# Kernel optimization log

Hardware: AMD Instinct MI355X
Metric: run time of the kernel (lower is better)

The kernel has to match this reference:

```python
import jax, jax.numpy as jnp
import numpy as np

V, D, H, HS, BLK, L = 50257, 768, 12, 64, 1024, 6
B, S = 4, 1024
EPS = 1e-5


def layer_norm(x, g, b):
    mu = jnp.mean(x, axis=-1, keepdims=True)
    var = jnp.mean(jnp.square(x - mu), axis=-1, keepdims=True)
    return (x - mu) * jax.lax.rsqrt(var + EPS) * g + b


def setup_inputs() -> dict:
    key = jax.random.key(0)
    ks = jax.random.split(key, 24)
    s = 0.02
    inp = {
        "idx": jax.random.randint(ks[0], (B, S), 0, V),
        "tok_emb": jax.random.normal(ks[1], (V, D), jnp.float32) * s,
        "pos_emb": jax.random.normal(ks[2], (BLK, D), jnp.float32) * s,
        "Wq": jax.random.normal(ks[3], (L, H, D, HS), jnp.float32) * s,
        "bq": jnp.zeros((L, H, HS), jnp.float32),
        "Wk": jax.random.normal(ks[4], (L, H, D, HS), jnp.float32) * s,
        "bk": jnp.zeros((L, H, HS), jnp.float32),
        "Wv": jax.random.normal(ks[5], (L, H, D, HS), jnp.float32) * s,
        "bv": jnp.zeros((L, H, HS), jnp.float32),
        "Wproj": jax.random.normal(ks[6], (L, D, D), jnp.float32) * s,
        "bproj": jnp.zeros((L, D), jnp.float32),
        "ln1_g": jnp.ones((L, D), jnp.float32),
        "ln1_b": jnp.zeros((L, D), jnp.float32),
        "ln2_g": jnp.ones((L, D), jnp.float32),
        "ln2_b": jnp.zeros((L, D), jnp.float32),
        "Wf1": jax.random.normal(ks[7], (L, D, 4 * D), jnp.float32) * s,
        "bf1": jnp.zeros((L, 4 * D), jnp.float32),
        "Wf2": jax.random.normal(ks[8], (L, 4 * D, D), jnp.float32) * s,
        "bf2": jnp.zeros((L, D), jnp.float32),
        "lnf_g": jnp.ones((D,), jnp.float32),
        "lnf_b": jnp.zeros((D,), jnp.float32),
        "Wlm": jax.random.normal(ks[9], (V, D), jnp.float32) * s,
    }
    return inp


def attention(x, Wq, bq, Wk, bk, Wv, bv, Wproj, bproj):
    # x: [B,S,D]; per-head projections stacked over H
    q = jnp.einsum("bsd,hdk->bhsk", x, Wq) + bq[:, None, :]
    k = jnp.einsum("bsd,hdk->bhsk", x, Wk) + bk[:, None, :]
    v = jnp.einsum("bsd,hdk->bhsk", x, Wv) + bv[:, None, :]
    scores = jnp.einsum("bhsk,bhtk->bhst", q, k)  # [B,H,S,S]
    s = x.shape[1]
    mask = jnp.tril(jnp.ones((s, s), bool))
    # original: masked_fill(-inf) THEN divide by sqrt(head_size) -- equivalent
    scores = jnp.where(mask, scores, -jnp.inf) / np.sqrt(HS)
    w = jax.nn.softmax(scores, axis=-1)
    out = jnp.einsum("bhst,bhtk->bhsk", w, v)
    out = out.transpose(0, 2, 1, 3).reshape(x.shape[0], s, H * HS)
    return out @ Wproj + bproj


def reference(idx, tok_emb, pos_emb, Wq, bq, Wk, bk, Wv, bv, Wproj, bproj,
              ln1_g, ln1_b, ln2_g, ln2_b, Wf1, bf1, Wf2, bf2, lnf_g, lnf_b, Wlm):
    s = idx.shape[1]
    x = tok_emb[idx] + pos_emb[:s]
    for i in range(L):
        h = layer_norm(x, ln1_g[i], ln1_b[i])
        x = x + attention(h, Wq[i], bq[i], Wk[i], bk[i], Wv[i], bv[i], Wproj[i], bproj[i])
        h = layer_norm(x, ln2_g[i], ln2_b[i])
        x = x + (jax.nn.gelu(h @ Wf1[i] + bf1[i], approximate=False) @ Wf2[i] + bf2[i])
    x = layer_norm(x, lnf_g, lnf_b)
    logits = x @ Wlm.T  # [B,S,V]
    return logits
```

## Files before the change

### kernel.cpp

```cpp
#include <hip/hip_runtime.h>
#include <hip/hip_bf16.h>
#include <math.h>

#define D_MODEL 768
#define N_HEAD  12
#define HEAD    64
#define SEQ     1024
#define NLAYER  6
#define BATCH   4
#define NROWS   (BATCH*SEQ)
#define VOCAB   50257
#define VPAD    50432
#define DFFN    3072
#define DQKV    2304

typedef __attribute__((ext_vector_type(8))) __bf16 bf16x8;
typedef __attribute__((ext_vector_type(4))) float f32x4;
typedef __attribute__((ext_vector_type(4))) unsigned short u16x4;

__device__ inline unsigned short f2bf(float x) {
    __hip_bfloat16 h = __float2bfloat16(x);
    return *reinterpret_cast<unsigned short*>(&h);
}

__global__ __launch_bounds__(256)
void embed_kernel(const int* __restrict__ idx, const float* __restrict__ tok,
                  const float* __restrict__ pos, float* __restrict__ x) {
    int row = blockIdx.x;
    int t = idx[row];
    int s = row & (SEQ - 1);
    const float* tp = tok + (size_t)t * D_MODEL;
    const float* pp = pos + (size_t)s * D_MODEL;
    float* xp = x + (size_t)row * D_MODEL;
    for (int i = threadIdx.x; i < D_MODEL; i += 256) xp[i] = tp[i] + pp[i];
}

__global__ __launch_bounds__(256)
void ln_kernel(const float* __restrict__ in, const float* __restrict__ gw,
               const float* __restrict__ bw, unsigned short* __restrict__ out) {
    int row = blockIdx.x;
    int tid = threadIdx.x;
    const float* x = in + (size_t)row * D_MODEL;
    float v0 = x[tid], v1 = x[tid + 256], v2 = x[tid + 512];
    float s  = v0 + v1 + v2;
    float sq = v0*v0 + v1*v1 + v2*v2;
    #pragma unroll
    for (int o = 1; o < 64; o <<= 1) { s += __shfl_xor(s, o); sq += __shfl_xor(sq, o); }
    __shared__ float red[8];
    int wave = tid >> 6;
    if ((tid & 63) == 0) { red[wave] = s; red[4 + wave] = sq; }
    __syncthreads();
    s  = red[0] + red[1] + red[2] + red[3];
    sq = red[4] + red[5] + red[6] + red[7];
    float mean = s * (1.0f / D_MODEL);
    float var  = sq * (1.0f / D_MODEL) - mean * mean;
    float rstd = rsqrtf(var + 1e-5f);
    unsigned short* op = out + (size_t)row * D_MODEL;
    op[tid]       = f2bf((v0 - mean) * rstd * gw[tid]       + bw[tid]);
    op[tid + 256] = f2bf((v1 - mean) * rstd * gw[tid + 256] + bw[tid + 256]);
    op[tid + 512] = f2bf((v2 - mean) * rstd * gw[tid + 512] + bw[tid + 512]);
}

template<int MODE>
__global__ __launch_bounds__(256)
void conv_transpose(const float* __restrict__ in, unsigned short* __restrict__ out,
                    int K, int N, size_t inLstride, size_t outLstride) {
    __shared__ float t[32][33];
    const int tx = threadIdx.x, ty = threadIdx.y;
    const int n0 = blockIdx.x * 32, k0 = blockIdx.y * 32;
    const float* ip = in + blockIdx.z * inLstride;
    unsigned short* op = out + blockIdx.z * outLstride;
    #pragma unroll
    for (int j = 0; j < 4; ++j) {
        int k = k0 + ty + j * 8, n = n0 + tx;
        float v = (MODE == 0) ? ip[(size_t)k * N + n]
                              : ip[(size_t)((n >> 6) * K + k) * 64 + (n & 63)];
        t[ty + j * 8][tx] = v;
    }
    __syncthreads();
    #pragma unroll
    for (int j = 0; j < 4; ++j) {
        int n = n0 + ty + j * 8, k = k0 + tx;
        op[(size_t)n * K + k] = f2bf(t[tx][ty + j * 8]);
    }
}

__global__ __launch_bounds__(256)
void conv_lm(const float* __restrict__ in, unsigned short* __restrict__ out) {
    const int nchunks = VPAD * D_MODEL / 4;
    const int vchunks = VOCAB * D_MODEL / 4;
    for (int i = blockIdx.x * 256 + threadIdx.x; i < nchunks; i += gridDim.x * 256) {
        u16x4 o;
        if (i < vchunks) {
            float4 v = reinterpret_cast<const float4*>(in)[i];
            o[0] = f2bf(v.x); o[1] = f2bf(v.y); o[2] = f2bf(v.z); o[3] = f2bf(v.w);
        } else { o[0] = 0; o[1] = 0; o[2] = 0; o[3] = 0; }
        reinterpret_cast<u16x4*>(out)[i] = o;
    }
}

__global__ __launch_bounds__(256)
void conv_bias(const float* __restrict__ bq, const float* __restrict__ bk,
               const float* __restrict__ bv, float* __restrict__ out) {
    int i = blockIdx.x * 256 + threadIdx.x;
    if (i >= NLAYER * DQKV) return;
    int l = i / DQKV, n = i % DQKV;
    float v;
    if (n < 768)        v = bq[l * 768 + n];
    else if (n < 1536)  v = bk[l * 768 + n - 768];
    else                v = bv[l * 768 + n - 1536];
    out[i] = v;
}

__global__ __launch_bounds__(512)
void gemm256_mfma(const unsigned short* __restrict__ A, const unsigned short* __restrict__ B,
                  float* __restrict__ C, int M, int N, int K) {
    __shared__ unsigned short smem[2 * 2 * 16384];
    const int nwg = gridDim.x;
    const int t0 = (blockIdx.x & 7) * (nwg >> 3) + (blockIdx.x >> 3);
    const int MT = M >> 8;
    const int NBX = nwg / MT;
    const int srsize = NBX * 8;
    const int sr = t0 / srsize;
    const int rem = t0 - sr * srsize;
    const int bx = rem >> 3;
    const int by = sr * 8 + (rem & 7);
    const int bm = by * 256, bn = bx * 256;
    const int tid = threadIdx.x;
    const int l = tid & 63, w = tid >> 6;
    const int wm = w >> 2, wn = w & 3;
    const int lr = l & 15, lc = l >> 4;
    f32x4 acc[8][4] = {};

    auto stage = [&](int k0, int buf) {
        #pragma unroll
        for (int p = 0; p < 4; ++p) {
            int d16 = p * 512 + tid;
            int row = d16 >> 3, cph = d16 & 7;
            int clog = cph ^ (row & 7);
            const unsigned short* ga = A + (size_t)(bm + row) * K + k0 + clog * 8;
            __builtin_amdgcn_global_load_lds(
                (const __attribute__((address_space(1))) unsigned int*)ga,
                (__attribute__((address_space(3))) unsigned int*)(&smem[buf * 32768 + d16 * 8]), 16, 0, 0);
        }
        #pragma unroll
        for (int p = 0; p < 4; ++p) {
            int d16 = p * 512 + tid;
            int row = d16 >> 3, cph = d16 & 7;
            int clog = cph ^ (row & 7);
            const unsigned short* gb = B + (size_t)(bn + row) * K + k0 + clog * 8;
            __builtin_amdgcn_global_load_lds(
                (const __attribute__((address_space(1))) unsigned int*)gb,
                (__attribute__((address_space(3))) unsigned int*)(&smem[buf * 32768 + 16384 + d16 * 8]), 16, 0, 0);
        }
    };

    auto compute = [&](int buf) {
        const unsigned short* Ab = &smem[buf * 32768];
        const unsigned short* Bb = &smem[buf * 32768 + 16384];
        #pragma unroll
        for (int qm = 0; qm < 2; ++qm) {
            bf16x8 af[2][4];
            #pragma unroll
            for (int ks = 0; ks < 2; ++ks)
                #pragma unroll
                for (int mi = 0; mi < 4; ++mi) {
                    int row = wm * 128 + qm * 64 + mi * 16 + lr;
                    af[ks][mi] = *reinterpret_cast<const bf16x8*>(
                        &Ab[row * 64 + (((ks * 4 + lc) ^ (row & 7)) * 8)]);
                }
            #pragma unroll
            for (int qn = 0; qn < 2; ++qn) {
                bf16x8 bfr[2][2];
                #pragma unroll
                for (int ks = 0; ks < 2; ++ks)
                    #pragma unroll
                    for (int ni = 0; ni < 2; ++ni) {
                        int col = wn * 64 + qn * 32 + ni * 16 + lr;
                        bfr[ks][ni] = *reinterpret_cast<const bf16x8*>(
                            &Bb[col * 64 + (((ks * 4 + lc) ^ (col & 7)) * 8)]);
                    }
                __builtin_amdgcn_s_setprio(1);
                #pragma unroll
                for (int ks = 0; ks < 2; ++ks)
                    #pragma unroll
                    for (int mi = 0; mi < 4; ++mi)
                        #pragma unroll
                        for (int ni = 0; ni < 2; ++ni)
                            acc[qm * 4 + mi][qn * 2 + ni] = __builtin_amdgcn_mfma_f32_16x16x32_bf16(
                                af[ks][mi], bfr[ks][ni], acc[qm * 4 + mi][qn * 2 + ni], 0, 0, 0);
                __builtin_amdgcn_s_setprio(0);
            }
        }
    };

    const int NT = K >> 6;
    stage(0, 0);
    asm volatile("s_waitcnt vmcnt(0)" ::: "memory");
    __builtin_amdgcn_s_barrier();
    for (int t = 0; t < NT; ++t) {
        const int cur = t & 1;
        if (t + 1 < NT) stage((t + 1) << 6, cur ^ 1);
        compute(cur);
        if (t + 1 < NT) {
            asm volatile("s_waitcnt vmcnt(0)" ::: "memory");
            __builtin_amdgcn_s_barrier();
        }
    }

    #pragma unroll
    for (int i = 0; i < 8; ++i) {
        #pragma unroll
        for (int r = 0; r < 4; ++r) {
            const int row = bm + wm * 128 + i * 16 + lc * 4 + r;
            #pragma unroll
            for (int j = 0; j < 4; ++j) {
                const int col = bn + wn * 64 + j * 16 + lr;
                if (col < N) C[(size_t)row * N + col] = acc[i][j][r];
            }
        }
    }
}

template<int OUTF , bool GELU, bool RES>
__global__ __launch_bounds__(256)
void gemm128p(const unsigned short* __restrict__ A, const unsigned short* __restrict__ B,
              const float* __restrict__ bias, const float* __restrict__ res,
              void* __restrict__ Cout, int M, int N, int K) {
    __shared__ unsigned short smem[2 * 2 * 8192];
    const int nwg = gridDim.x;
    const int t0 = (blockIdx.x & 7) * (nwg >> 3) + (blockIdx.x >> 3);
    const int MT = M >> 7;
    const int NBX = nwg / MT;
    const int srsize = NBX * 8;
    const int sr = t0 / srsize;
    const int rem = t0 - sr * srsize;
    const int bx = rem >> 3;
    const int by = sr * 8 + (rem & 7);
    const int bm = by * 128, bn = bx * 128;
    const int tid = threadIdx.x;
    const int l = tid & 63, w = tid >> 6;
    const int wr = (w >> 1) * 64, wc = (w & 1) * 64;
    const int lr = l & 15, lc = l >> 4;
    f32x4 acc[4][4] = {};

    auto stage = [&](int k0, int buf) {
        #pragma unroll
        for (int p = 0; p < 4; ++p) {
            int d16 = p * 256 + tid;
            int row = d16 >> 3, cph = d16 & 7;
            int clog = cph ^ (row & 7);
            const unsigned short* ga = A + (size_t)(bm + row) * K + k0 + clog * 8;
            __builtin_amdgcn_global_load_lds(
                (const __attribute__((address_space(1))) unsigned int*)ga,
                (__attribute__((address_space(3))) unsigned int*)(&smem[buf * 16384 + d16 * 8]), 16, 0, 0);
        }
        #pragma unroll
        for (int p = 0; p < 4; ++p) {
            int d16 = p * 256 + tid;
            int row = d16 >> 3, cph = d16 & 7;
            int clog = cph ^ (row & 7);
            const unsigned short* gb = B + (size_t)(bn + row) * K + k0 + clog * 8;
            __builtin_amdgcn_global_load_lds(
                (const __attribute__((address_space(1))) unsigned int*)gb,
                (__attribute__((address_space(3))) unsigned int*)(&smem[buf * 16384 + 8192 + d16 * 8]), 16, 0, 0);
        }
    };

    auto compute = [&](int buf) {
        const unsigned short* Ab = &smem[buf * 16384];
        const unsigned short* Bb = &smem[buf * 16384 + 8192];
        #pragma unroll
        for (int ks = 0; ks < 2; ++ks) {
            bf16x8 af[4], bfr[4];
            #pragma unroll
            for (int mi = 0; mi < 4; ++mi) {
                int row = wr + mi * 16 + lr;
                af[mi] = *reinterpret_cast<const bf16x8*>(
                    &Ab[row * 64 + (((ks * 4 + lc) ^ (row & 7)) * 8)]);
            }
            #pragma unroll
            for (int ni = 0; ni < 4; ++ni) {
                int col = wc + ni * 16 + lr;
                bfr[ni] = *reinterpret_cast<const bf16x8*>(
                    &Bb[col * 64 + (((ks * 4 + lc) ^ (col & 7)) * 8)]);
            }
            __builtin_amdgcn_s_setprio(1);
            #pragma unroll
            for (int mi = 0; mi < 4; ++mi)
                #pragma unroll
                for (int ni = 0; ni < 4; ++ni)
                    acc[mi][ni] = __builtin_amdgcn_mfma_f32_16x16x32_bf16(
                        af[mi], bfr[ni], acc[mi][ni], 0, 0, 0);
            __builtin_amdgcn_s_setprio(0);
        }
    };

    const int NT = K >> 6;
    stage(0, 0);
    asm volatile("s_waitcnt vmcnt(0)" ::: "memory");
    __builtin_amdgcn_s_barrier();
    for (int t = 0; t < NT; ++t) {
        const int cur = t & 1;
        if (t + 1 < NT) stage((t + 1) << 6, cur ^ 1);
        compute(cur);
        if (t + 1 < NT) {
            asm volatile("s_waitcnt vmcnt(0)" ::: "memory");
            __builtin_amdgcn_s_barrier();
        }
    }

    #pragma unroll
    for (int mi = 0; mi < 4; ++mi) {
        #pragma unroll
        for (int r = 0; r < 4; ++r) {
            const int row = bm + wr + mi * 16 + lc * 4 + r;
            #pragma unroll
            for (int ni = 0; ni < 4; ++ni) {
                const int col = bn + wc + ni * 16 + lr;
                float v = acc[mi][ni][r];
                if (bias) v += bias[col];
                if (GELU) v = 0.5f * v * (1.0f + erff(v * 0.70710678118654752f));
                if (RES)  v += res[(size_t)row * N + col];
                if (OUTF == 0) ((float*)Cout)[(size_t)row * N + col] = v;
                else ((unsigned short*)Cout)[(size_t)row * N + col] = f2bf(v);
            }
        }
    }
}

__global__ __launch_bounds__(256)
void attn_mfma(const unsigned short* __restrict__ qkv, unsigned short* __restrict__ ao) {
    const int qt = gridDim.x - 1 - blockIdx.x;
    const int h = blockIdx.y, b = blockIdx.z;
    const int tid = threadIdx.x;
    const int w = tid >> 6, l = tid & 63;
    const int c = l & 15, g = l >> 4;

    __shared__ unsigned short Ks[32 * 64];
    __shared__ unsigned short Vt[64 * 40];
    __shared__ unsigned int   Ps[4][16 * 20];

    const unsigned short* base = qkv + (size_t)(b * SEQ) * DQKV + h * HEAD;
    const int q0 = qt * 64 + w * 16;

    bf16x8 qf[2];
    {
        const unsigned short* qp = base + (size_t)(q0 + c) * DQKV + g * 8;
        qf[0] = *reinterpret_cast<const bf16x8*>(qp);
        qf[1] = *reinterpret_cast<const bf16x8*>(qp + 32);
    }

    f32x4 o_acc[4] = {};
    float m_run[4]  = {-INFINITY, -INFINITY, -INFINITY, -INFINITY};
    float l_run[4]  = {0.f, 0.f, 0.f, 0.f};

    const int srow = tid >> 3, schunk = tid & 7;
    const int vd = tid & 63, vw = tid >> 6;

    const int nkt = 2 * qt + 2;
    for (int kt = 0; kt < nkt; ++kt) {
        {
            const unsigned short* kp = base + (size_t)(kt * 32 + srow) * DQKV + 768 + schunk * 8;
            bf16x8 kv = *reinterpret_cast<const bf16x8*>(kp);
            *reinterpret_cast<bf16x8*>(&Ks[srow * 64 + ((schunk ^ (srow & 7)) * 8)]) = kv;
        }
        {
            unsigned short vv[8];
            #pragma unroll
            for (int j = 0; j < 8; ++j)
                vv[j] = base[(size_t)(kt * 32 + vw * 8 + j) * DQKV + 1536 + vd];
            uint4 pk;
            pk.x = vv[0] | ((unsigned)vv[1] << 16);
            pk.y = vv[2] | ((unsigned)vv[3] << 16);
            pk.z = vv[4] | ((unsigned)vv[5] << 16);
            pk.w = vv[6] | ((unsigned)vv[7] << 16);
            *reinterpret_cast<uint4*>(&Vt[vd * 40 + vw * 8]) = pk;
        }
        __syncthreads();

        f32x4 s_acc[2] = {};
        #pragma unroll
        for (int t = 0; t < 2; ++t) {
            const int kr = t * 16 + c;
            #pragma unroll
            for (int ks = 0; ks < 2; ++ks) {
                bf16x8 kf = *reinterpret_cast<const bf16x8*>(
                    &Ks[kr * 64 + (((ks * 4 + g) ^ (kr & 7)) * 8)]);
                s_acc[t] = __builtin_amdgcn_mfma_f32_16x16x32_bf16(qf[ks], kf, s_acc[t], 0, 0, 0);
            }
        }
        float sc[2][4];
        #pragma unroll
        for (int t = 0; t < 2; ++t) {
            const int kglob = kt * 32 + t * 16 + c;
            #pragma unroll
            for (int r = 0; r < 4; ++r) {
                float v = s_acc[t][r] * 0.125f;
                sc[t][r] = (kglob > q0 + g * 4 + r) ? -1e30f : v;
            }
        }
        float pout[2][4];
        #pragma unroll
        for (int r = 0; r < 4; ++r) {
            float tmax = fmaxf(sc[0][r], sc[1][r]);
            #pragma unroll
            for (int ms = 1; ms < 16; ms <<= 1) tmax = fmaxf(tmax, __shfl_xor(tmax, ms));
            float mnew = fmaxf(m_run[r], tmax);
            float alpha = __expf(m_run[r] - mnew);
            float p0 = __expf(sc[0][r] - mnew);
            float p1 = __expf(sc[1][r] - mnew);
            float psum = p0 + p1;
            #pragma unroll
            for (int ms = 1; ms < 16; ms <<= 1) psum += __shfl_xor(psum, ms);
            l_run[r] = l_run[r] * alpha + psum;
            m_run[r] = mnew;
            #pragma unroll
            for (int dt = 0; dt < 4; ++dt) o_acc[dt][r] *= alpha;
            pout[0][r] = p0; pout[1][r] = p1;
        }
        #pragma unroll
        for (int t = 0; t < 2; ++t) {
            #pragma unroll
            for (int r = 0; r < 4; ++r) {
                int my = f2bf(pout[t][r]);
                int part = __shfl_xor(my, 1);
                unsigned int word = (c & 1) ? ((unsigned)(part & 0xffff) | ((unsigned)my << 16))
                                            : ((unsigned)(my & 0xffff) | ((unsigned)part << 16));
                Ps[w][(g * 4 + r) * 20 + t * 8 + (c >> 1)] = word;
            }
        }
        uint4 praw = *reinterpret_cast<const uint4*>(&Ps[w][c * 20 + g * 4]);
        bf16x8 pf = *reinterpret_cast<const bf16x8*>(&praw);
        #pragma unroll
        for (int dt = 0; dt < 4; ++dt) {
            bf16x8 vf = *reinterpret_cast<const bf16x8*>(&Vt[(dt * 16 + c) * 40 + g * 8]);
            o_acc[dt] = __builtin_amdgcn_mfma_f32_16x16x32_bf16(pf, vf, o_acc[dt], 0, 0, 0);
        }
        __syncthreads();
    }

    float inv[4];
    #pragma unroll
    for (int r = 0; r < 4; ++r) inv[r] = 1.0f / l_run[r];
    #pragma unroll
    for (int r = 0; r < 4; ++r) {
        unsigned short* op = ao + (size_t)(b * SEQ + q0 + g * 4 + r) * D_MODEL + h * HEAD + c;
        #pragma unroll
        for (int dt = 0; dt < 4; ++dt)
            op[dt * 16] = f2bf(o_acc[dt][r] * inv[r]);
    }
}

extern "C" void kernel_launch(void* const* d_in, const int* in_sizes, int n_in,
                              void* d_out, int out_size, void* d_ws, size_t ws_size,
                              hipStream_t stream) {
    const int*   idx     = (const int*)  d_in[0];
    const float* tok_emb = (const float*)d_in[1];
    const float* pos_emb = (const float*)d_in[2];
    const float* Wq      = (const float*)d_in[3];
    const float* bq      = (const float*)d_in[4];
    const float* Wk      = (const float*)d_in[5];
    const float* bk      = (const float*)d_in[6];
    const float* Wv      = (const float*)d_in[7];
    const float* bv      = (const float*)d_in[8];
    const float* Wproj   = (const float*)d_in[9];
    const float* bproj   = (const float*)d_in[10];
    const float* ln1g    = (const float*)d_in[11];
    const float* ln1b    = (const float*)d_in[12];
    const float* ln2g    = (const float*)d_in[13];
    const float* ln2b    = (const float*)d_in[14];
    const float* Wf1     = (const float*)d_in[15];
    const float* bf1     = (const float*)d_in[16];
    const float* Wf2     = (const float*)d_in[17];
    const float* bf2     = (const float*)d_in[18];
    const float* lnfg    = (const float*)d_in[19];
    const float* lnfb    = (const float*)d_in[20];
    const float* Wlm     = (const float*)d_in[21];
    float* outp = (float*)d_out;

    char* basep = (char*)d_ws;
    size_t off = 0;
    auto alloc = [&](size_t bytes) -> void* {
        void* p = basep + off;
        off = (off + bytes + 255) & ~(size_t)255;
        return p;
    };
    float*          x      = (float*)         alloc((size_t)NROWS * D_MODEL * 4);
    unsigned short* qkv    = (unsigned short*)alloc((size_t)NROWS * DQKV * 2);
    unsigned short* hb     = (unsigned short*)alloc((size_t)NROWS * D_MODEL * 2);
    unsigned short* ao     = (unsigned short*)alloc((size_t)NROWS * D_MODEL * 2);
    unsigned short* mid    = (unsigned short*)alloc((size_t)NROWS * DFFN * 2);
    unsigned short* Wqkvb  = (unsigned short*)alloc((size_t)NLAYER * DQKV * D_MODEL * 2);
    unsigned short* Wprojb = (unsigned short*)alloc((size_t)NLAYER * D_MODEL * D_MODEL * 2);
    unsigned short* Wf1b   = (unsigned short*)alloc((size_t)NLAYER * DFFN * D_MODEL * 2);
    unsigned short* Wf2b   = (unsigned short*)alloc((size_t)NLAYER * D_MODEL * DFFN * 2);
    unsigned short* Wlmb   = (unsigned short*)alloc((size_t)VPAD * D_MODEL * 2);
    float*          bqkv   = (float*)         alloc((size_t)NLAYER * DQKV * 4);

    dim3 blk(256);
    dim3 tblk(32, 8);

    conv_lm<<<2048, blk, 0, stream>>>(Wlm, Wlmb);
    conv_transpose<1><<<dim3(24, 24, 6), tblk, 0, stream>>>(Wq, Wqkvb,             768, 768,  (size_t)768*768,  (size_t)DQKV*768);
    conv_transpose<1><<<dim3(24, 24, 6), tblk, 0, stream>>>(Wk, Wqkvb + 768*768,   768, 768,  (size_t)768*768,  (size_t)DQKV*768);
    conv_transpose<1><<<dim3(24, 24, 6), tblk, 0, stream>>>(Wv, Wqkvb + 2*768*768, 768, 768,  (size_t)768*768,  (size_t)DQKV*768);
    conv_transpose<0><<<dim3(24, 24, 6), tblk, 0, stream>>>(Wproj, Wprojb,         768, 768,  (size_t)768*768,  (size_t)768*768);
    conv_transpose<0><<<dim3(96, 24, 6), tblk, 0, stream>>>(Wf1, Wf1b,             768, 3072, (size_t)768*3072, (size_t)3072*768);
    conv_transpose<0><<<dim3(24, 96, 6), tblk, 0, stream>>>(Wf2, Wf2b,             3072, 768, (size_t)3072*768, (size_t)768*3072);
    conv_bias<<<(NLAYER * DQKV + 255) / 256, blk, 0, stream>>>(bq, bk, bv, bqkv);

    embed_kernel<<<NROWS, blk, 0, stream>>>(idx, tok_emb, pos_emb, x);

    dim3 gqkv(32 * 18);
    dim3 g768(32 * 6);
    dim3 g3072(32 * 24);
    dim3 ga(SEQ / 64, N_HEAD, BATCH);

    for (int li = 0; li < NLAYER; ++li) {
        ln_kernel<<<NROWS, blk, 0, stream>>>(x, ln1g + li * D_MODEL, ln1b + li * D_MODEL, hb);

        gemm128p<1, false, false><<<gqkv, blk, 0, stream>>>(
            hb, Wqkvb + (size_t)li * DQKV * D_MODEL, bqkv + li * DQKV, nullptr,
            qkv, NROWS, DQKV, D_MODEL);

        attn_mfma<<<ga, blk, 0, stream>>>(qkv, ao);

        gemm128p<0, false, true><<<g768, blk, 0, stream>>>(
            ao, Wprojb + (size_t)li * D_MODEL * D_MODEL, bproj + li * D_MODEL, x,
            x, NROWS, D_MODEL, D_MODEL);

        ln_kernel<<<NROWS, blk, 0, stream>>>(x, ln2g + li * D_MODEL, ln2b + li * D_MODEL, hb);

        gemm128p<1, true, false><<<g3072, blk, 0, stream>>>(
            hb, Wf1b + (size_t)li * DFFN * D_MODEL, bf1 + li * DFFN, nullptr,
            mid, NROWS, DFFN, D_MODEL);

        gemm128p<0, false, true><<<g768, blk, 0, stream>>>(
            mid, Wf2b + (size_t)li * D_MODEL * DFFN, bf2 + li * D_MODEL, x,
            x, NROWS, D_MODEL, DFFN);
    }

    ln_kernel<<<NROWS, blk, 0, stream>>>(x, lnfg, lnfb, hb);

    dim3 gl((VPAD / 256) * (NROWS / 256));
    gemm256_mfma<<<gl, dim3(512), 0, stream>>>(hb, Wlmb, outp, NROWS, VOCAB, D_MODEL);
}
```

Baseline: 2.336 ms.

## Use 64-row tiles for N=768 GEMMs and 512-thread attention blocks

Templates the GEMM on the M tile size. The two N=768 residual GEMMs (proj and FFN2) now use 64x128 tiles, which doubles the workgroup count from 192 to 384 and fills more CUs. Attention blocks grow to 8 waves covering 128 query rows, so each K/V tile staged in shared memory is reused by twice as many queries. Each thread now loads half-width K/V chunks. The cost is more causal-mask waste per block and smaller per-wave MFMA tiles in the 64-row GEMM.

```diff
diff --git a/kernel.cpp b/kernel.cpp
--- a/kernel.cpp
+++ b/kernel.cpp
@@ -222,38 +222,42 @@
     }
 }
 
-template<int OUTF , bool GELU, bool RES>
+template<int BM, int OUTF , bool GELU, bool RES>
 __global__ __launch_bounds__(256)
-void gemm128p(const unsigned short* __restrict__ A, const unsigned short* __restrict__ B,
-              const float* __restrict__ bias, const float* __restrict__ res,
-              void* __restrict__ Cout, int M, int N, int K) {
-    __shared__ unsigned short smem[2 * 2 * 8192];
+void gemm_sched(const unsigned short* __restrict__ A, const unsigned short* __restrict__ B,
+                const float* __restrict__ bias, const float* __restrict__ res,
+                void* __restrict__ Cout, int M, int N, int K) {
+    constexpr int ABUF = BM * 64;
+    constexpr int TBUF = (BM + 128) * 64;
+    __shared__ unsigned short smem[2 * TBUF];
     const int nwg = gridDim.x;
     const int t0 = (blockIdx.x & 7) * (nwg >> 3) + (blockIdx.x >> 3);
-    const int MT = M >> 7;
+    const int MT = M / BM;
     const int NBX = nwg / MT;
     const int srsize = NBX * 8;
     const int sr = t0 / srsize;
     const int rem = t0 - sr * srsize;
     const int bx = rem >> 3;
     const int by = sr * 8 + (rem & 7);
-    const int bm = by * 128, bn = bx * 128;
+    const int bm = by * BM, bn = bx * 128;
     const int tid = threadIdx.x;
     const int l = tid & 63, w = tid >> 6;
-    const int wr = (w >> 1) * 64, wc = (w & 1) * 64;
+    constexpr int MI = (BM == 128) ? 4 : 2;
+    const int wr = (BM == 128) ? (w >> 1) * 64 : (w & 1) * 32;
+    const int wc = (BM == 128) ? (w & 1) * 64 : (w >> 1) * 64;
     const int lr = l & 15, lc = l >> 4;
-    f32x4 acc[4][4] = {};
+    f32x4 acc[MI][4] = {};
 
     auto stage = [&](int k0, int buf) {
         #pragma unroll
-        for (int p = 0; p < 4; ++p) {
+        for (int p = 0; p < BM * 8 / 256; ++p) {
             int d16 = p * 256 + tid;
             int row = d16 >> 3, cph = d16 & 7;
             int clog = cph ^ (row & 7);
             const unsigned short* ga = A + (size_t)(bm + row) * K + k0 + clog * 8;
             __builtin_amdgcn_global_load_lds(
                 (const __attribute__((address_space(1))) unsigned int*)ga,
-                (__attribute__((address_space(3))) unsigned int*)(&smem[buf * 16384 + d16 * 8]), 16, 0, 0);
+                (__attribute__((address_space(3))) unsigned int*)(&smem[buf * TBUF + d16 * 8]), 16, 0, 0);
         }
         #pragma unroll
         for (int p = 0; p < 4; ++p) {
@@ -263,18 +267,18 @@
             const unsigned short* gb = B + (size_t)(bn + row) * K + k0 + clog * 8;
             __builtin_amdgcn_global_load_lds(
                 (const __attribute__((address_space(1))) unsigned int*)gb,
-                (__attribute__((address_space(3))) unsigned int*)(&smem[buf * 16384 + 8192 + d16 * 8]), 16, 0, 0);
+                (__attribute__((address_space(3))) unsigned int*)(&smem[buf * TBUF + ABUF + d16 * 8]), 16, 0, 0);
         }
     };
 
     auto compute = [&](int buf) {
-        const unsigned short* Ab = &smem[buf * 16384];
-        const unsigned short* Bb = &smem[buf * 16384 + 8192];
+        const unsigned short* Ab = &smem[buf * TBUF];
+        const unsigned short* Bb = &smem[buf * TBUF + ABUF];
         #pragma unroll
         for (int ks = 0; ks < 2; ++ks) {
-            bf16x8 af[4], bfr[4];
-            #pragma unroll
-            for (int mi = 0; mi < 4; ++mi) {
+            bf16x8 af[MI], bfr[4];
+            #pragma unroll
+            for (int mi = 0; mi < MI; ++mi) {
                 int row = wr + mi * 16 + lr;
                 af[mi] = *reinterpret_cast<const bf16x8*>(
                     &Ab[row * 64 + (((ks * 4 + lc) ^ (row & 7)) * 8)]);
@@ -287,7 +291,7 @@
             }
             __builtin_amdgcn_s_setprio(1);
             #pragma unroll
-            for (int mi = 0; mi < 4; ++mi)
+            for (int mi = 0; mi < MI; ++mi)
                 #pragma unroll
                 for (int ni = 0; ni < 4; ++ni)
                     acc[mi][ni] = __builtin_amdgcn_mfma_f32_16x16x32_bf16(
@@ -311,7 +315,7 @@
     }
 
     #pragma unroll
-    for (int mi = 0; mi < 4; ++mi) {
+    for (int mi = 0; mi < MI; ++mi) {
         #pragma unroll
         for (int r = 0; r < 4; ++r) {
             const int row = bm + wr + mi * 16 + lc * 4 + r;
@@ -329,7 +333,7 @@
     }
 }
 
-__global__ __launch_bounds__(256)
+__global__ __launch_bounds__(512)
 void attn_mfma(const unsigned short* __restrict__ qkv, unsigned short* __restrict__ ao) {
     const int qt = gridDim.x - 1 - blockIdx.x;
     const int h = blockIdx.y, b = blockIdx.z;
@@ -339,10 +343,10 @@
 
     __shared__ unsigned short Ks[32 * 64];
     __shared__ unsigned short Vt[64 * 40];
-    __shared__ unsigned int   Ps[4][16 * 20];
+    __shared__ unsigned int   Ps[8][16 * 20];
 
     const unsigned short* base = qkv + (size_t)(b * SEQ) * DQKV + h * HEAD;
-    const int q0 = qt * 64 + w * 16;
+    const int q0 = qt * 128 + w * 16;
 
     bf16x8 qf[2];
     {
@@ -355,27 +359,26 @@
     float m_run[4]  = {-INFINITY, -INFINITY, -INFINITY, -INFINITY};
     float l_run[4]  = {0.f, 0.f, 0.f, 0.f};
 
-    const int srow = tid >> 3, schunk = tid & 7;
+    const int srow = tid >> 4, sch8 = tid & 15;
+    const int scj = sch8 >> 1, sh = sch8 & 1;
     const int vd = tid & 63, vw = tid >> 6;
 
-    const int nkt = 2 * qt + 2;
+    const int nkt = 4 * qt + 4;
     for (int kt = 0; kt < nkt; ++kt) {
         {
-            const unsigned short* kp = base + (size_t)(kt * 32 + srow) * DQKV + 768 + schunk * 8;
-            bf16x8 kv = *reinterpret_cast<const bf16x8*>(kp);
-            *reinterpret_cast<bf16x8*>(&Ks[srow * 64 + ((schunk ^ (srow & 7)) * 8)]) = kv;
+            const unsigned short* kp = base + (size_t)(kt * 32 + srow) * DQKV + 768 + sch8 * 4;
+            u16x4 kv = *reinterpret_cast<const u16x4*>(kp);
+            *reinterpret_cast<u16x4*>(&Ks[srow * 64 + ((scj ^ (srow & 7)) * 8) + sh * 4]) = kv;
         }
         {
-            unsigned short vv[8];
-            #pragma unroll
-            for (int j = 0; j < 8; ++j)
-                vv[j] = base[(size_t)(kt * 32 + vw * 8 + j) * DQKV + 1536 + vd];
-            uint4 pk;
+            unsigned short vv[4];
+            #pragma unroll
+            for (int j = 0; j < 4; ++j)
+                vv[j] = base[(size_t)(kt * 32 + vw * 4 + j) * DQKV + 1536 + vd];
+            uint2 pk;
             pk.x = vv[0] | ((unsigned)vv[1] << 16);
             pk.y = vv[2] | ((unsigned)vv[3] << 16);
-            pk.z = vv[4] | ((unsigned)vv[5] << 16);
-            pk.w = vv[6] | ((unsigned)vv[7] << 16);
-            *reinterpret_cast<uint4*>(&Vt[vd * 40 + vw * 8]) = pk;
+            *reinterpret_cast<uint2*>(&Vt[vd * 40 + vw * 4]) = pk;
         }
         __syncthreads();
 
@@ -513,30 +516,30 @@
     embed_kernel<<<NROWS, blk, 0, stream>>>(idx, tok_emb, pos_emb, x);
 
     dim3 gqkv(32 * 18);
-    dim3 g768(32 * 6);
+    dim3 g768s(64 * 6);
     dim3 g3072(32 * 24);
-    dim3 ga(SEQ / 64, N_HEAD, BATCH);
+    dim3 ga(SEQ / 128, N_HEAD, BATCH);
 
     for (int li = 0; li < NLAYER; ++li) {
         ln_kernel<<<NROWS, blk, 0, stream>>>(x, ln1g + li * D_MODEL, ln1b + li * D_MODEL, hb);
 
-        gemm128p<1, false, false><<<gqkv, blk, 0, stream>>>(
+        gemm_sched<128, 1, false, false><<<gqkv, blk, 0, stream>>>(
             hb, Wqkvb + (size_t)li * DQKV * D_MODEL, bqkv + li * DQKV, nullptr,
             qkv, NROWS, DQKV, D_MODEL);
 
-        attn_mfma<<<ga, blk, 0, stream>>>(qkv, ao);
-
-        gemm128p<0, false, true><<<g768, blk, 0, stream>>>(
+        attn_mfma<<<ga, dim3(512), 0, stream>>>(qkv, ao);
+
+        gemm_sched<64, 0, false, true><<<g768s, blk, 0, stream>>>(
             ao, Wprojb + (size_t)li * D_MODEL * D_MODEL, bproj + li * D_MODEL, x,
             x, NROWS, D_MODEL, D_MODEL);
 
         ln_kernel<<<NROWS, blk, 0, stream>>>(x, ln2g + li * D_MODEL, ln2b + li * D_MODEL, hb);
 
-        gemm128p<1, true, false><<<g3072, blk, 0, stream>>>(
+        gemm_sched<128, 1, true, false><<<g3072, blk, 0, stream>>>(
             hb, Wf1b + (size_t)li * DFFN * D_MODEL, bf1 + li * DFFN, nullptr,
             mid, NROWS, DFFN, D_MODEL);
 
-        gemm128p<0, false, true><<<g768, blk, 0, stream>>>(
+        gemm_sched<64, 0, false, true><<<g768s, blk, 0, stream>>>(
             mid, Wf2b + (size_t)li * D_MODEL * DFFN, bf2 + li * D_MODEL, x,
             x, NROWS, D_MODEL, DFFN);
     }
```

Result: faster. 2.267 ms (-3.0%).
